# Kernel tuning notes

Measured on AMD Instinct MI355X. Metric: run time of the kernel, lower is better.

## Reference

```python
import jax, jax.numpy as jnp
import numpy as np

QP_ITERS = 500          # projected-gradient iterations on the dual (converges for this tiny QP)
S_PEN = 1000.0          # slack penalty from the cvxpy objective
BN_EPS = 1e-5


def batchnorm(x, gamma, beta):
    # x: (B, N, C); BatchNorm1d training-mode stats over (batch, points)
    mu = x.mean(axis=(0, 1))
    var = x.var(axis=(0, 1))
    return (x - mu) * jax.lax.rsqrt(var + BN_EPS) * gamma + beta


def solve_qp(p, G, h):
    # min_z,s 0.5||z-p||^2 + 1000||s||^2  s.t. G z <= h + s, s >= 0
    # Dual (eliminating z = p - G^T lam, s = lam/(2*1000)):
    #   min_{lam>=0} 0.5 lam^T M lam - lam^T q,  M = G G^T + I/(2*S_PEN), q = G p - h
    nc = G.shape[1]
    M = jnp.einsum('bcv,bdv->bcd', G, G) + jnp.eye(nc, dtype=G.dtype) / (2.0 * S_PEN)
    q = jnp.einsum('bcv,bv->bc', G, p) - h
    # safe step size: 1/trace(M) <= 1/lambda_max(M)
    alpha = jax.lax.stop_gradient(1.0 / jnp.trace(M, axis1=1, axis2=2))[:, None]

    def step(lam, _):
        grad = jnp.einsum('bcd,bd->bc', M, lam) - q
        return jnp.maximum(lam - alpha * grad, 0.0), None

    lam0 = jnp.zeros_like(q)
    lam, _ = jax.lax.scan(step, lam0, None, length=QP_ITERS)
    z = p - jnp.einsum('bcv,bc->bv', G, lam)
    return z


def setup_inputs() -> dict:
    key = jax.random.key(0)
    ks = jax.random.split(key, 16)
    B, N, NC = 64, 8192, 12

    def w(k, shape, s):
        return (jax.random.normal(k, shape) * s).astype(jnp.float32)

    bc2 = jnp.concatenate([w(ks[10], (NC * 3,), 0.02), jnp.full((NC,), 0.02, jnp.float32)])
    return {
        'pcd': jax.random.normal(ks[0], (B, N, 3), dtype=jnp.float32),
        # MiniPointNet (1x1 convs as matmuls) + batchnorm affine params
        'W1': w(ks[1], (64, 3), 0.4), 'b1': jnp.zeros(64), 'g1': jnp.ones(64), 'be1': jnp.zeros(64),
        'W2': w(ks[2], (128, 64), 0.1), 'b2': jnp.zeros(128), 'g2': jnp.ones(128), 'be2': jnp.zeros(128),
        'W3': w(ks[3], (256, 128), 0.07), 'b3': jnp.zeros(256), 'g3': jnp.ones(256), 'be3': jnp.zeros(256),
        'Wfc': w(ks[4], (128, 256), 0.05), 'bfc': jnp.zeros(128),
        # constraint_net: 128 -> 128 -> 48
        'Wc1': w(ks[5], (128, 128), 0.08), 'bc1': jnp.zeros(128),
        'Wc2': w(ks[6], (NC * 4, 128), 0.08), 'bc2': bc2,
        # p_net: 128 -> 64 -> 7 (last layer ~N(0, 0.001), zero bias)
        'Wp1': w(ks[7], (64, 128), 0.08), 'bp1': jnp.zeros(64),
        'Wp2': w(ks[8], (7, 64), 0.001), 'bp2': jnp.zeros(7),
    }


def reference(pcd, W1, b1, g1, be1, W2, b2, g2, be2, W3, b3, g3, be3,
              Wfc, bfc, Wc1, bc1, Wc2, bc2, Wp1, bp1, Wp2, bp2):
    B = pcd.shape[0]
    NC = bc2.shape[0] // 4
    # MiniPointNet: pointwise MLP + global max pool
    x = jax.nn.relu(batchnorm(pcd @ W1.T + b1, g1, be1))     # (B,N,64)
    x = jax.nn.relu(batchnorm(x @ W2.T + b2, g2, be2))       # (B,N,128)
    x = jax.nn.relu(batchnorm(x @ W3.T + b3, g3, be3))       # (B,N,256)
    feats = x.max(axis=1) @ Wfc.T + bfc                       # (B,128)

    raw_p = jax.nn.relu(feats @ Wp1.T + bp1) @ Wp2.T + bp2    # (B,7)
    p_pred = jnp.concatenate([
        jnp.tanh(raw_p[:, :3]) * 0.1,
        jnp.tanh(raw_p[:, 3:6]) * 1.57,
        jnp.tanh(raw_p[:, 6:7]) * 0.05], axis=1)

    out_cons = (jax.nn.relu(feats @ Wc1.T + bc1) @ Wc2.T + bc2).reshape(B, NC, 4)
    normals = out_cons[:, :, :3]
    # F.normalize(p=2, dim=2): clamp norm at 1e-12
    normals = normals / jnp.clip(jnp.linalg.norm(normals, axis=2, keepdims=True), 1e-12)
    h = jax.nn.softplus(out_cons[:, :, 3]) + 0.005            # (B,NC)
    G = jnp.concatenate([normals, jnp.zeros((B, NC, 4), normals.dtype)], axis=2)  # (B,NC,7)

    delta_norm = solve_qp(p_pred, G, h)                       # (B,7)
    return delta_norm, normals, h, p_pred
```

## Files before the change

kernel.cpp:

```cpp
#include <hip/hip_runtime.h>
#include <hip/hip_bf16.h>

#define NPTS 524288
#define NBATCH 64
#define NSAMP 131072

typedef __attribute__((ext_vector_type(8))) short bf16x8;
typedef __attribute__((ext_vector_type(4))) float f32x4;
typedef const float* __restrict__ fp;

__device__ __forceinline__ __hip_bfloat16 f2b(float v) { return __float2bfloat16(v); }
__device__ __forceinline__ unsigned bfbits(float v) {
    union { __hip_bfloat16 h; unsigned short s; } u; u.h = f2b(v); return (unsigned)u.s;
}
__device__ __forceinline__ unsigned pk2(float a, float b) {
    return bfbits(a) | (bfbits(b) << 16);
}
__device__ __forceinline__ float lo2f(unsigned u) { return __uint_as_float(u << 16); }
__device__ __forceinline__ float hi2f(unsigned u) { return __uint_as_float(u & 0xffff0000u); }

__device__ __forceinline__ unsigned fkey(float f) {
    unsigned u = __float_as_uint(f);
    return u ^ ((u & 0x80000000u) ? 0xFFFFFFFFu : 0x80000000u);
}
__device__ __forceinline__ float funkey(unsigned k) {
    unsigned u = (k & 0x80000000u) ? (k ^ 0x80000000u) : ~k;
    return __uint_as_float(u);
}

union U8 { bf16x8 v; __hip_bfloat16 e[8]; unsigned u[4]; };

static __device__ __forceinline__ f32x4 mfma16(bf16x8 a, bf16x8 b, f32x4 c) {
    return __builtin_amdgcn_mfma_f32_16x16x32_bf16(a, b, c, 0, 0, 0);
}

__launch_bounds__(256)
__global__ void k_setup(fp pcd, float* __restrict__ mom,
                        fp W2, fp W3, __hip_bfloat16* __restrict__ W2b,
                        __hip_bfloat16* __restrict__ W3b)
{
    if (blockIdx.x >= 1024) {
        const int i = (blockIdx.x - 1024) * 256 + threadIdx.x;
        if (i < 8192) W2b[i] = f2b(W2[i]);
        const int j = i - 8192;
        if (j >= 0 && j < 32768) W3b[j] = f2b(W3[j]);
        return;
    }
    float s[9];
#pragma unroll
    for (int i = 0; i < 9; ++i) s[i] = 0.f;
    for (int p = blockIdx.x * 256 + threadIdx.x; p < NPTS; p += 262144) {
        const float x = pcd[3*p+0], y = pcd[3*p+1], z = pcd[3*p+2];
        s[0] += x; s[1] += y; s[2] += z;
        s[3] = fmaf(x, x, s[3]); s[4] = fmaf(x, y, s[4]); s[5] = fmaf(x, z, s[5]);
        s[6] = fmaf(y, y, s[6]); s[7] = fmaf(y, z, s[7]); s[8] = fmaf(z, z, s[8]);
    }
#pragma unroll
    for (int off = 1; off < 64; off <<= 1) {
#pragma unroll
        for (int i = 0; i < 9; ++i) s[i] += __shfl_xor(s[i], off);
    }
    __shared__ float red[4][9];
    const int lane = threadIdx.x & 63, wv = threadIdx.x >> 6;
    if (lane == 0) {
#pragma unroll
        for (int i = 0; i < 9; ++i) red[wv][i] = s[i];
    }
    __syncthreads();
    if (threadIdx.x < 9) {
        const int i = threadIdx.x;
        atomicAdd(&mom[i], red[0][i] + red[1][i] + red[2][i] + red[3][i]);
    }
}

__global__ void k_fin1(const float* __restrict__ mom, fp W1, fp b1, fp g1, fp be1,
                       unsigned* __restrict__ W1p)
{
    const int c = threadIdx.x;
    const float inv = 1.f / (float)NPTS;
    const float m0 = mom[0]*inv, m1 = mom[1]*inv, m2 = mom[2]*inv;
    const float c00 = mom[3]*inv - m0*m0, c01 = mom[4]*inv - m0*m1, c02 = mom[5]*inv - m0*m2;
    const float c11 = mom[6]*inv - m1*m1, c12 = mom[7]*inv - m1*m2, c22 = mom[8]*inv - m2*m2;
    const float w0 = W1[c*3+0], w1 = W1[c*3+1], w2 = W1[c*3+2];
    const float mu = w0*m0 + w1*m1 + w2*m2 + b1[c];
    float var = w0*w0*c00 + w1*w1*c11 + w2*w2*c22 + 2.f*(w0*w1*c01 + w0*w2*c02 + w1*w2*c12);
    var = fmaxf(var, 0.f);
    const float sc = g1[c] * rsqrtf(var + 1e-5f);
    const float sh = be1[c] - mu*sc;
    W1p[c*2+0] = pk2(w0*sc, w1*sc);
    W1p[c*2+1] = pk2(w2*sc, b1[c]*sc + sh);
}

#define L1_DIRECT(a2f, px, py, pz)                                              \
    {                                                                           \
        _Pragma("unroll")                                                       \
        for (int ks = 0; ks < 2; ++ks) {                                        \
            _Pragma("unroll")                                                   \
            for (int t2 = 0; t2 < 4; ++t2) {                                    \
                const int t0 = ks*8 + 2*t2;                                     \
                float v0 = fmaf(px, lo2f(wA[t0]), hi2f(wB[t0]));                \
                v0 = fmaf(py, hi2f(wA[t0]), v0);                                \
                v0 = fmaf(pz, lo2f(wB[t0]), v0);                                \
                float v1 = fmaf(px, lo2f(wA[t0+1]), hi2f(wB[t0+1]));            \
                v1 = fmaf(py, hi2f(wA[t0+1]), v1);                              \
                v1 = fmaf(pz, lo2f(wB[t0+1]), v1);                              \
                a2f[ks].u[t2] = pk2(fmaxf(v0, 0.f), fmaxf(v1, 0.f));            \
            }                                                                   \
        }                                                                       \
    }

#define LOAD_W1()                                                               \
    unsigned wA[16], wB[16];                                                    \
    _Pragma("unroll")                                                           \
    for (int t = 0; t < 16; ++t) {                                              \
        const int ch = (t >> 3)*32 + q*8 + (t & 7);                             \
        wA[t] = W1p[ch*2]; wB[t] = W1p[ch*2+1];                                 \
    }

__launch_bounds__(256, 3)
__global__ void k_pass1(fp pcd, const unsigned* __restrict__ W1p,
                        const __hip_bfloat16* __restrict__ W2b,
                        float* __restrict__ st2s, float* __restrict__ st2q)
{
    __shared__ float red[1024];
    const int tid = threadIdx.x, wv = tid >> 6, lane = tid & 63;
    const int m = lane & 15, q = lane >> 4;
    const int batch = blockIdx.x >> 3, sub = blockIdx.x & 7;

    LOAD_W1()
    bf16x8 wb2[8][2];
#pragma unroll
    for (int nt = 0; nt < 8; ++nt) {
#pragma unroll
        for (int kk = 0; kk < 2; ++kk)
            wb2[nt][kk] = *(const bf16x8*)(W2b + (nt*16+m)*64 + kk*32 + q*8);
    }

    float s_acc[8], q_acc[8];
#pragma unroll
    for (int nt = 0; nt < 8; ++nt) { s_acc[nt] = 0.f; q_acc[nt] = 0.f; }

#pragma unroll
    for (int it = 0; it < 4; ++it) {
        const int p0 = batch*8192 + sub*1024 + it*256 + wv*16;
        const float* pp = pcd + (size_t)(p0 + m) * 3;
        const float px = pp[0], py = pp[1], pz = pp[2];
        U8 a2f[2];
        L1_DIRECT(a2f, px, py, pz)
#pragma unroll
        for (int nt = 0; nt < 8; ++nt) {
            f32x4 c = mfma16(a2f[0].v, wb2[nt][0], (f32x4){0.f,0.f,0.f,0.f});
            c = mfma16(a2f[1].v, wb2[nt][1], c);
            s_acc[nt] += (c[0] + c[1]) + (c[2] + c[3]);
            q_acc[nt] = fmaf(c[0],c[0], fmaf(c[1],c[1], fmaf(c[2],c[2], fmaf(c[3],c[3], q_acc[nt]))));
        }
    }
#pragma unroll
    for (int nt = 0; nt < 8; ++nt) {
        s_acc[nt] += __shfl_xor(s_acc[nt], 16); q_acc[nt] += __shfl_xor(q_acc[nt], 16);
        s_acc[nt] += __shfl_xor(s_acc[nt], 32); q_acc[nt] += __shfl_xor(q_acc[nt], 32);
    }
    if (q == 0) {
#pragma unroll
        for (int nt = 0; nt < 8; ++nt) {
            red[wv*128 + nt*16 + m] = s_acc[nt];
            red[512 + wv*128 + nt*16 + m] = q_acc[nt];
        }
    }
    __syncthreads();
    if (tid < 128) {
        float s = 0.f, ss = 0.f;
#pragma unroll
        for (int w4 = 0; w4 < 4; ++w4) { s += red[w4*128 + tid]; ss += red[512 + w4*128 + tid]; }
        const int slot = blockIdx.x & 63;
        atomicAdd(&st2s[slot*128 + tid], s);
        atomicAdd(&st2q[slot*128 + tid], ss);
    }
}

__global__ void k_fin2(const float* __restrict__ sum, const float* __restrict__ sq,
                       fp W2, fp g, fp be,
                       float* __restrict__ tOut, __hip_bfloat16* __restrict__ W2s)
{
    const int ch = threadIdx.x;
    float s = 0.f, ss = 0.f;
    for (int slot = 0; slot < 64; ++slot) { s += sum[slot*128 + ch]; ss += sq[slot*128 + ch]; }
    const float inv = 1.f / (float)NSAMP;
    const float mu = s * inv;
    const float var = fmaxf(ss * inv - mu*mu, 0.f);
    const float sc = g[ch] * rsqrtf(var + 1e-5f);
    tOut[ch] = be[ch] - mu*sc;
    for (int k = 0; k < 64; ++k) W2s[ch*64 + k] = f2b(sc * W2[ch*64 + k]);
}

__launch_bounds__(256)
__global__ void k_pass2(fp pcd, const unsigned* __restrict__ W1p,
                        const __hip_bfloat16* __restrict__ W2s,
                        const float* __restrict__ t2,
                        const __hip_bfloat16* __restrict__ W3b,
                        float* __restrict__ st3s, float* __restrict__ st3q,
                        unsigned* __restrict__ maxk, unsigned* __restrict__ mink)
{
    __shared__ alignas(16) __hip_bfloat16 x2s[128*136];
    __shared__ alignas(16) __hip_bfloat16 w2s[128*72];
    const int tid = threadIdx.x, wv = tid >> 6, lane = tid & 63;
    const int m = lane & 15, q = lane >> 4;
    const int batch = blockIdx.x >> 5, sub = blockIdx.x & 31;

    {
        const int row = tid >> 1, half = tid & 1;
#pragma unroll
        for (int jj = 0; jj < 2; ++jj) {
            const bf16x8 wa = *(const bf16x8*)(W2s + row*64 + half*32 + jj*16);
            const bf16x8 wb = *(const bf16x8*)(W2s + row*64 + half*32 + jj*16 + 8);
            *(bf16x8*)&w2s[row*72 + half*32 + jj*16]     = wa;
            *(bf16x8*)&w2s[row*72 + half*32 + jj*16 + 8] = wb;
        }
    }

    LOAD_W1()
    float t2v[8];
#pragma unroll
    for (int nt = 0; nt < 8; ++nt) t2v[nt] = t2[nt*16+m];

    bf16x8 wb3[4][4];
#pragma unroll
    for (int nt = 0; nt < 4; ++nt) {
        const int ch3 = wv*64 + nt*16 + m;
#pragma unroll
        for (int ks = 0; ks < 4; ++ks)
            wb3[nt][ks] = *(const bf16x8*)(W3b + ch3*128 + ks*32 + q*8);
    }

    float s3[4], q3[4], mx3[4], mn3[4];
#pragma unroll
    for (int nt = 0; nt < 4; ++nt) { s3[nt]=0.f; q3[nt]=0.f; mx3[nt]=-3.4e38f; mn3[nt]=3.4e38f; }

    __syncthreads();

#pragma unroll
    for (int half = 0; half < 2; ++half) {
        if (half) __syncthreads();
#pragma unroll
        for (int it = 0; it < 2; ++it) {
            const int p0 = batch*8192 + sub*256 + (half*2+it)*64 + wv*16;
            const float* pp = pcd + (size_t)(p0 + m) * 3;
            const float px = pp[0], py = pp[1], pz = pp[2];
            U8 a2f[2];
            L1_DIRECT(a2f, px, py, pz)
#pragma unroll
            for (int nt = 0; nt < 8; ++nt) {
                const bf16x8 wb20 = *(const bf16x8*)&w2s[(nt*16+m)*72 + 0  + q*8];
                const bf16x8 wb21 = *(const bf16x8*)&w2s[(nt*16+m)*72 + 32 + q*8];
                f32x4 c = mfma16(a2f[0].v, wb20, (f32x4){0.f,0.f,0.f,0.f});
                c = mfma16(a2f[1].v, wb21, c);
#pragma unroll
                for (int r = 0; r < 4; ++r) {
                    const float v = fmaxf(c[r] + t2v[nt], 0.f);
                    const unsigned own = bfbits(v);
                    const unsigned oth = (unsigned)__shfl_xor((int)own, 1);
                    if ((m & 1) == 0) {
                        const int row = it*64 + wv*16 + q*4 + r;
                        *(unsigned*)&x2s[row*136 + nt*16 + m] = own | (oth << 16);
                    }
                }
            }
        }
        __syncthreads();
        for (int ms = 0; ms < 8; ++ms) {
            const int rowM = (ms*16 + m) * 136;
            bf16x8 a3[4];
#pragma unroll
            for (int ks = 0; ks < 4; ++ks)
                a3[ks] = *(const bf16x8*)&x2s[rowM + ks*32 + q*8];
#pragma unroll
            for (int nt = 0; nt < 4; ++nt) {
                f32x4 c = mfma16(a3[0], wb3[nt][0], (f32x4){0.f,0.f,0.f,0.f});
                c = mfma16(a3[1], wb3[nt][1], c);
                c = mfma16(a3[2], wb3[nt][2], c);
                c = mfma16(a3[3], wb3[nt][3], c);
                s3[nt] += (c[0] + c[1]) + (c[2] + c[3]);
                q3[nt] = fmaf(c[0],c[0], fmaf(c[1],c[1], fmaf(c[2],c[2], fmaf(c[3],c[3], q3[nt]))));
                mx3[nt] = fmaxf(fmaxf(c[0], c[1]), fmaxf(fmaxf(c[2], c[3]), mx3[nt]));
                mn3[nt] = fminf(fminf(c[0], c[1]), fminf(fminf(c[2], c[3]), mn3[nt]));
            }
        }
    }
#pragma unroll
    for (int nt = 0; nt < 4; ++nt) {
        s3[nt] += __shfl_xor(s3[nt], 16);  q3[nt] += __shfl_xor(q3[nt], 16);
        mx3[nt] = fmaxf(mx3[nt], __shfl_xor(mx3[nt], 16));
        mn3[nt] = fminf(mn3[nt], __shfl_xor(mn3[nt], 16));
        s3[nt] += __shfl_xor(s3[nt], 32);  q3[nt] += __shfl_xor(q3[nt], 32);
        mx3[nt] = fmaxf(mx3[nt], __shfl_xor(mx3[nt], 32));
        mn3[nt] = fminf(mn3[nt], __shfl_xor(mn3[nt], 32));
    }
    if (q == 0) {
        const int slot = blockIdx.x & 63;
#pragma unroll
        for (int nt = 0; nt < 4; ++nt) {
            const int ch3 = wv*64 + nt*16 + m;
            atomicAdd(&st3s[slot*256 + ch3], s3[nt]);
            atomicAdd(&st3q[slot*256 + ch3], q3[nt]);
            atomicMax(&maxk[batch*256 + ch3], fkey(mx3[nt]));
            atomicMin(&mink[batch*256 + ch3], fkey(mn3[nt]));
        }
    }
}

__launch_bounds__(128)
__global__ void k_head(const float* __restrict__ st3s, const float* __restrict__ st3q,
                       fp g3, fp be3,
                       const unsigned* __restrict__ maxk, const unsigned* __restrict__ mink,
                       fp Wfc, fp bfc, fp Wc1, fp bc1, fp Wc2, fp bc2,
                       fp Wp1, fp bp1, fp Wp2, fp bp2,
                       float* __restrict__ out)
{
    __shared__ float pf[256], ft[128], hcs[128], hps[64], ocs[48], nrm[36], hS[12], pp[8];
    const int bb = blockIdx.x, tid = threadIdx.x;
#pragma unroll
    for (int h = 0; h < 2; ++h) {
        const int ch = tid + h*128;
        float s = 0.f, ss = 0.f;
        for (int slot = 0; slot < 64; ++slot) { s += st3s[slot*256 + ch]; ss += st3q[slot*256 + ch]; }
        const float inv = 1.f / (float)NPTS;
        const float mu = s * inv;
        const float var = fmaxf(ss * inv - mu*mu, 0.f);
        const float sc = g3[ch] * rsqrtf(var + 1e-5f);
        const float sh = be3[ch] - mu*sc;
        const float pick = (sc >= 0.f) ? funkey(maxk[bb*256 + ch]) : funkey(mink[bb*256 + ch]);
        pf[ch] = fmaxf(fmaf(pick, sc, sh), 0.f);
    }
    __syncthreads();
    {
        float a = bfc[tid];
        const float* wr = Wfc + tid*256;
        for (int k = 0; k < 256; ++k) a = fmaf(pf[k], wr[k], a);
        ft[tid] = a;
    }
    __syncthreads();
    {
        float a = bc1[tid];
        const float* wr = Wc1 + tid*128;
        for (int k = 0; k < 128; ++k) a = fmaf(ft[k], wr[k], a);
        hcs[tid] = fmaxf(a, 0.f);
    }
    if (tid < 64) {
        float a = bp1[tid];
        const float* wr = Wp1 + tid*128;
        for (int k = 0; k < 128; ++k) a = fmaf(ft[k], wr[k], a);
        hps[tid] = fmaxf(a, 0.f);
    }
    __syncthreads();
    if (tid < 48) {
        float a = bc2[tid];
        const float* wr = Wc2 + tid*128;
        for (int k = 0; k < 128; ++k) a = fmaf(hcs[k], wr[k], a);
        ocs[tid] = a;
    }
    if (tid < 7) {
        float a = bp2[tid];
        const float* wr = Wp2 + tid*64;
        for (int k = 0; k < 64; ++k) a = fmaf(hps[k], wr[k], a);
        const float sc = (tid < 3) ? 0.1f : ((tid < 6) ? 1.57f : 0.05f);
        pp[tid] = tanhf(a) * sc;
    }
    __syncthreads();
    if (tid < 12) {
        float nx = ocs[tid*4+0], ny = ocs[tid*4+1], nz = ocs[tid*4+2];
        const float nn = fmaxf(sqrtf(nx*nx + ny*ny + nz*nz), 1e-12f);
        const float inv = 1.f / nn;
        nx *= inv; ny *= inv; nz *= inv;
        nrm[tid*3+0] = nx; nrm[tid*3+1] = ny; nrm[tid*3+2] = nz;
        const float xx = ocs[tid*4+3];
        hS[tid] = ((xx > 20.f) ? xx : log1pf(expf(xx))) + 0.005f;
    }
    __syncthreads();

    const int lane = tid & 63;
    const int c = (lane < 12) ? lane : 11;
    const float n0 = nrm[c*3+0], n1 = nrm[c*3+1], n2 = nrm[c*3+2];
    float Mrow[12];
    float trace = 0.f;
#pragma unroll
    for (int d = 0; d < 12; ++d) {
        const float d0 = nrm[d*3+0], d1 = nrm[d*3+1], d2 = nrm[d*3+2];
        Mrow[d] = n0*d0 + n1*d1 + n2*d2 + ((d == lane) ? 5e-4f : 0.f);
        trace += d0*d0 + d1*d1 + d2*d2;
    }
    const float alpha = 1.f / (trace + 12.f*5e-4f);
    const float qc = n0*pp[0] + n1*pp[1] + n2*pp[2] - hS[c];
    float lam = 0.f;
    for (int it = 0; it < 500; ++it) {
        const float l0 = __shfl(lam, 0),  l1 = __shfl(lam, 1),  l2 = __shfl(lam, 2);
        const float l3 = __shfl(lam, 3),  l4 = __shfl(lam, 4),  l5 = __shfl(lam, 5);
        const float l6 = __shfl(lam, 6),  l7 = __shfl(lam, 7),  l8 = __shfl(lam, 8);
        const float l9 = __shfl(lam, 9),  l10 = __shfl(lam, 10), l11 = __shfl(lam, 11);
        const float g0 = fmaf(Mrow[0], l0, fmaf(Mrow[3], l3, fmaf(Mrow[6], l6, Mrow[9]*l9)));
        const float g1 = fmaf(Mrow[1], l1, fmaf(Mrow[4], l4, fmaf(Mrow[7], l7, Mrow[10]*l10)));
        const float g2 = fmaf(Mrow[2], l2, fmaf(Mrow[5], l5, fmaf(Mrow[8], l8, Mrow[11]*l11)));
        lam = fmaxf(fmaf(-alpha, g0 + g1 + g2 - qc, lam), 0.f);
    }
    float v0 = (lane < 12) ? n0*lam : 0.f;
    float v1 = (lane < 12) ? n1*lam : 0.f;
    float v2 = (lane < 12) ? n2*lam : 0.f;
#pragma unroll
    for (int off = 1; off <= 8; off <<= 1) {
        v0 += __shfl_xor(v0, off);
        v1 += __shfl_xor(v1, off);
        v2 += __shfl_xor(v2, off);
    }
    if (tid < 7) {
        float z;
        if (tid == 0) z = pp[0] - v0;
        else if (tid == 1) z = pp[1] - v1;
        else if (tid == 2) z = pp[2] - v2;
        else z = pp[tid];
        out[bb*7 + tid] = z;
    }
    if (tid < 36) out[448 + bb*36 + tid] = nrm[tid];
    if (tid < 12) out[2752 + bb*12 + tid] = hS[tid];
    if (tid < 7)  out[3520 + bb*7 + tid] = pp[tid];
}

extern "C" void kernel_launch(void* const* d_in, const int* in_sizes, int n_in,
                              void* d_out, int out_size, void* d_ws, size_t ws_size,
                              hipStream_t stream) {
    fp pcd = (fp)d_in[0];
    fp W1 = (fp)d_in[1],  b1 = (fp)d_in[2],  g1 = (fp)d_in[3],  be1 = (fp)d_in[4];
    fp W2 = (fp)d_in[5],  g2 = (fp)d_in[7],  be2 = (fp)d_in[8];
    fp W3 = (fp)d_in[9],  g3 = (fp)d_in[11], be3 = (fp)d_in[12];
    fp Wfc = (fp)d_in[13], bfc = (fp)d_in[14];
    fp Wc1 = (fp)d_in[15], bc1 = (fp)d_in[16];
    fp Wc2 = (fp)d_in[17], bc2 = (fp)d_in[18];
    fp Wp1 = (fp)d_in[19], bp1 = (fp)d_in[20];
    fp Wp2 = (fp)d_in[21], bp2 = (fp)d_in[22];

    float* ws = (float*)d_ws;
    float* mom  = ws + 0;
    float* t2   = ws + 272;
    float* st2s = ws + 400;
    float* st2q = ws + 8592;
    float* st3s = ws + 16784;
    float* st3q = ws + 33168;
    unsigned* maxk = (unsigned*)(ws + 49552);
    unsigned* mink = (unsigned*)(ws + 65936);
    __hip_bfloat16* W2b = (__hip_bfloat16*)(ws + 82320);
    __hip_bfloat16* W3b = (__hip_bfloat16*)(ws + 86416);
    unsigned* W1p = (unsigned*)(ws + 102800);
    __hip_bfloat16* W2s = (__hip_bfloat16*)(ws + 102928);
    if (ws_size < (size_t)107024 * 4) return;

    hipMemsetAsync(d_ws, 0, (size_t)65936 * 4, stream);
    hipMemsetAsync((void*)mink, 0xFF, (size_t)16384 * 4, stream);

    k_setup<<<1184, 256, 0, stream>>>(pcd, mom, W2, W3, W2b, W3b);
    k_fin1<<<1, 64, 0, stream>>>(mom, W1, b1, g1, be1, W1p);
    k_pass1<<<512, 256, 0, stream>>>(pcd, W1p, W2b, st2s, st2q);
    k_fin2<<<1, 128, 0, stream>>>(st2s, st2q, W2, g2, be2, t2, W2s);
    k_pass2<<<2048, 256, 0, stream>>>(pcd, W1p, W2s, t2, W3b,
                                      st3s, st3q, maxk, mink);
    k_head<<<64, 128, 0, stream>>>(st3s, st3q, g3, be3, maxk, mink,
                                   Wfc, bfc, Wc1, bc1, Wc2, bc2,
                                   Wp1, bp1, Wp2, bp2, (float*)d_out);
}
```

Baseline: 330.8 us.

## Fold BN3 gamma sign into W3 to drop min tracking; keep W2 in registers

Pre-multiplies W3 rows by the sign of gamma3 so the layer-3 max pool only needs per-channel maxima, removing min tracking, the min atomics and the extra memset. W2 fragments are now held in registers instead of being staged through LDS. All 256 point rows are buffered in LDS before layer 3 to remove an intermediate barrier, and launch bounds request two blocks per CU. This trades higher VGPR and LDS use for fewer atomics, fewer LDS reads and fewer syncs.

```diff
diff --git a/kernel.cpp b/kernel.cpp
--- a/kernel.cpp
+++ b/kernel.cpp
@@ -36,14 +36,18 @@
 
 __launch_bounds__(256)
 __global__ void k_setup(fp pcd, float* __restrict__ mom,
-                        fp W2, fp W3, __hip_bfloat16* __restrict__ W2b,
+                        fp W2, fp W3, fp g3,
+                        __hip_bfloat16* __restrict__ W2b,
                         __hip_bfloat16* __restrict__ W3b)
 {
     if (blockIdx.x >= 1024) {
         const int i = (blockIdx.x - 1024) * 256 + threadIdx.x;
         if (i < 8192) W2b[i] = f2b(W2[i]);
         const int j = i - 8192;
-        if (j >= 0 && j < 32768) W3b[j] = f2b(W3[j]);
+        if (j >= 0 && j < 32768) {
+            const float s = (g3[j >> 7] < 0.f) ? -1.f : 1.f;
+            W3b[j] = f2b(s * W3[j]);
+        }
         return;
     }
     float s[9];
@@ -193,32 +197,27 @@
     for (int k = 0; k < 64; ++k) W2s[ch*64 + k] = f2b(sc * W2[ch*64 + k]);
 }
 
-__launch_bounds__(256)
+__launch_bounds__(256, 2)
 __global__ void k_pass2(fp pcd, const unsigned* __restrict__ W1p,
                         const __hip_bfloat16* __restrict__ W2s,
                         const float* __restrict__ t2,
                         const __hip_bfloat16* __restrict__ W3b,
                         float* __restrict__ st3s, float* __restrict__ st3q,
-                        unsigned* __restrict__ maxk, unsigned* __restrict__ mink)
-{
-    __shared__ alignas(16) __hip_bfloat16 x2s[128*136];
-    __shared__ alignas(16) __hip_bfloat16 w2s[128*72];
+                        unsigned* __restrict__ maxk)
+{
+    __shared__ alignas(16) __hip_bfloat16 x2s[256*136];
     const int tid = threadIdx.x, wv = tid >> 6, lane = tid & 63;
     const int m = lane & 15, q = lane >> 4;
     const int batch = blockIdx.x >> 5, sub = blockIdx.x & 31;
 
-    {
-        const int row = tid >> 1, half = tid & 1;
-#pragma unroll
-        for (int jj = 0; jj < 2; ++jj) {
-            const bf16x8 wa = *(const bf16x8*)(W2s + row*64 + half*32 + jj*16);
-            const bf16x8 wb = *(const bf16x8*)(W2s + row*64 + half*32 + jj*16 + 8);
-            *(bf16x8*)&w2s[row*72 + half*32 + jj*16]     = wa;
-            *(bf16x8*)&w2s[row*72 + half*32 + jj*16 + 8] = wb;
-        }
-    }
-
     LOAD_W1()
+    bf16x8 wb2[8][2];
+#pragma unroll
+    for (int nt = 0; nt < 8; ++nt) {
+#pragma unroll
+        for (int kk = 0; kk < 2; ++kk)
+            wb2[nt][kk] = *(const bf16x8*)(W2s + (nt*16+m)*64 + kk*32 + q*8);
+    }
     float t2v[8];
 #pragma unroll
     for (int nt = 0; nt < 8; ++nt) t2v[nt] = t2[nt*16+m];
@@ -232,68 +231,58 @@
             wb3[nt][ks] = *(const bf16x8*)(W3b + ch3*128 + ks*32 + q*8);
     }
 
-    float s3[4], q3[4], mx3[4], mn3[4];
-#pragma unroll
-    for (int nt = 0; nt < 4; ++nt) { s3[nt]=0.f; q3[nt]=0.f; mx3[nt]=-3.4e38f; mn3[nt]=3.4e38f; }
-
-    __syncthreads();
-
-#pragma unroll
-    for (int half = 0; half < 2; ++half) {
-        if (half) __syncthreads();
-#pragma unroll
-        for (int it = 0; it < 2; ++it) {
-            const int p0 = batch*8192 + sub*256 + (half*2+it)*64 + wv*16;
-            const float* pp = pcd + (size_t)(p0 + m) * 3;
-            const float px = pp[0], py = pp[1], pz = pp[2];
-            U8 a2f[2];
-            L1_DIRECT(a2f, px, py, pz)
-#pragma unroll
-            for (int nt = 0; nt < 8; ++nt) {
-                const bf16x8 wb20 = *(const bf16x8*)&w2s[(nt*16+m)*72 + 0  + q*8];
-                const bf16x8 wb21 = *(const bf16x8*)&w2s[(nt*16+m)*72 + 32 + q*8];
-                f32x4 c = mfma16(a2f[0].v, wb20, (f32x4){0.f,0.f,0.f,0.f});
-                c = mfma16(a2f[1].v, wb21, c);
-#pragma unroll
-                for (int r = 0; r < 4; ++r) {
-                    const float v = fmaxf(c[r] + t2v[nt], 0.f);
-                    const unsigned own = bfbits(v);
-                    const unsigned oth = (unsigned)__shfl_xor((int)own, 1);
-                    if ((m & 1) == 0) {
-                        const int row = it*64 + wv*16 + q*4 + r;
-                        *(unsigned*)&x2s[row*136 + nt*16 + m] = own | (oth << 16);
-                    }
+#pragma unroll
+    for (int it = 0; it < 4; ++it) {
+        const int p0 = batch*8192 + sub*256 + it*64 + wv*16;
+        const float* pp = pcd + (size_t)(p0 + m) * 3;
+        const float px = pp[0], py = pp[1], pz = pp[2];
+        U8 a2f[2];
+        L1_DIRECT(a2f, px, py, pz)
+#pragma unroll
+        for (int nt = 0; nt < 8; ++nt) {
+            f32x4 c = mfma16(a2f[0].v, wb2[nt][0], (f32x4){0.f,0.f,0.f,0.f});
+            c = mfma16(a2f[1].v, wb2[nt][1], c);
+#pragma unroll
+            for (int r = 0; r < 4; ++r) {
+                const float v = fmaxf(c[r] + t2v[nt], 0.f);
+                const unsigned own = bfbits(v);
+                const unsigned oth = (unsigned)__shfl_xor((int)own, 1);
+                if ((m & 1) == 0) {
+                    const int row = it*64 + wv*16 + q*4 + r;
+                    *(unsigned*)&x2s[row*136 + nt*16 + m] = own | (oth << 16);
                 }
             }
         }
-        __syncthreads();
-        for (int ms = 0; ms < 8; ++ms) {
-            const int rowM = (ms*16 + m) * 136;
-            bf16x8 a3[4];
-#pragma unroll
-            for (int ks = 0; ks < 4; ++ks)
-                a3[ks] = *(const bf16x8*)&x2s[rowM + ks*32 + q*8];
-#pragma unroll
-            for (int nt = 0; nt < 4; ++nt) {
-                f32x4 c = mfma16(a3[0], wb3[nt][0], (f32x4){0.f,0.f,0.f,0.f});
-                c = mfma16(a3[1], wb3[nt][1], c);
-                c = mfma16(a3[2], wb3[nt][2], c);
-                c = mfma16(a3[3], wb3[nt][3], c);
-                s3[nt] += (c[0] + c[1]) + (c[2] + c[3]);
-                q3[nt] = fmaf(c[0],c[0], fmaf(c[1],c[1], fmaf(c[2],c[2], fmaf(c[3],c[3], q3[nt]))));
-                mx3[nt] = fmaxf(fmaxf(c[0], c[1]), fmaxf(fmaxf(c[2], c[3]), mx3[nt]));
-                mn3[nt] = fminf(fminf(c[0], c[1]), fminf(fminf(c[2], c[3]), mn3[nt]));
-            }
+    }
+    __syncthreads();
+
+    float s3[4], q3[4], mx3[4];
+#pragma unroll
+    for (int nt = 0; nt < 4; ++nt) { s3[nt]=0.f; q3[nt]=0.f; mx3[nt]=-3.4e38f; }
+
+    for (int ms = 0; ms < 16; ++ms) {
+        const int rowM = (ms*16 + m) * 136;
+        bf16x8 a3[4];
+#pragma unroll
+        for (int ks = 0; ks < 4; ++ks)
+            a3[ks] = *(const bf16x8*)&x2s[rowM + ks*32 + q*8];
+#pragma unroll
+        for (int nt = 0; nt < 4; ++nt) {
+            f32x4 c = mfma16(a3[0], wb3[nt][0], (f32x4){0.f,0.f,0.f,0.f});
+            c = mfma16(a3[1], wb3[nt][1], c);
+            c = mfma16(a3[2], wb3[nt][2], c);
+            c = mfma16(a3[3], wb3[nt][3], c);
+            s3[nt] += (c[0] + c[1]) + (c[2] + c[3]);
+            q3[nt] = fmaf(c[0],c[0], fmaf(c[1],c[1], fmaf(c[2],c[2], fmaf(c[3],c[3], q3[nt]))));
+            mx3[nt] = fmaxf(fmaxf(c[0], c[1]), fmaxf(fmaxf(c[2], c[3]), mx3[nt]));
         }
     }
 #pragma unroll
     for (int nt = 0; nt < 4; ++nt) {
         s3[nt] += __shfl_xor(s3[nt], 16);  q3[nt] += __shfl_xor(q3[nt], 16);
         mx3[nt] = fmaxf(mx3[nt], __shfl_xor(mx3[nt], 16));
-        mn3[nt] = fminf(mn3[nt], __shfl_xor(mn3[nt], 16));
         s3[nt] += __shfl_xor(s3[nt], 32);  q3[nt] += __shfl_xor(q3[nt], 32);
         mx3[nt] = fmaxf(mx3[nt], __shfl_xor(mx3[nt], 32));
-        mn3[nt] = fminf(mn3[nt], __shfl_xor(mn3[nt], 32));
     }
     if (q == 0) {
         const int slot = blockIdx.x & 63;
@@ -303,15 +292,13 @@
             atomicAdd(&st3s[slot*256 + ch3], s3[nt]);
             atomicAdd(&st3q[slot*256 + ch3], q3[nt]);
             atomicMax(&maxk[batch*256 + ch3], fkey(mx3[nt]));
-            atomicMin(&mink[batch*256 + ch3], fkey(mn3[nt]));
         }
     }
 }
 
 __launch_bounds__(128)
 __global__ void k_head(const float* __restrict__ st3s, const float* __restrict__ st3q,
-                       fp g3, fp be3,
-                       const unsigned* __restrict__ maxk, const unsigned* __restrict__ mink,
+                       fp g3, fp be3, const unsigned* __restrict__ maxk,
                        fp Wfc, fp bfc, fp Wc1, fp bc1, fp Wc2, fp bc2,
                        fp Wp1, fp bp1, fp Wp2, fp bp2,
                        float* __restrict__ out)
@@ -326,10 +313,9 @@
         const float inv = 1.f / (float)NPTS;
         const float mu = s * inv;
         const float var = fmaxf(ss * inv - mu*mu, 0.f);
-        const float sc = g3[ch] * rsqrtf(var + 1e-5f);
-        const float sh = be3[ch] - mu*sc;
-        const float pick = (sc >= 0.f) ? funkey(maxk[bb*256 + ch]) : funkey(mink[bb*256 + ch]);
-        pf[ch] = fmaxf(fmaf(pick, sc, sh), 0.f);
+        const float asc = fabsf(g3[ch]) * rsqrtf(var + 1e-5f);
+        const float mx = funkey(maxk[bb*256 + ch]);
+        pf[ch] = fmaxf(fmaf(asc, mx - mu, be3[ch]), 0.f);
     }
     __syncthreads();
     {
@@ -444,7 +430,6 @@
     float* st3s = ws + 16784;
     float* st3q = ws + 33168;
     unsigned* maxk = (unsigned*)(ws + 49552);
-    unsigned* mink = (unsigned*)(ws + 65936);
     __hip_bfloat16* W2b = (__hip_bfloat16*)(ws + 82320);
     __hip_bfloat16* W3b = (__hip_bfloat16*)(ws + 86416);
     unsigned* W1p = (unsigned*)(ws + 102800);
@@ -452,15 +437,14 @@
     if (ws_size < (size_t)107024 * 4) return;
 
     hipMemsetAsync(d_ws, 0, (size_t)65936 * 4, stream);
-    hipMemsetAsync((void*)mink, 0xFF, (size_t)16384 * 4, stream);
-
-    k_setup<<<1184, 256, 0, stream>>>(pcd, mom, W2, W3, W2b, W3b);
+
+    k_setup<<<1184, 256, 0, stream>>>(pcd, mom, W2, W3, g3, W2b, W3b);
     k_fin1<<<1, 64, 0, stream>>>(mom, W1, b1, g1, be1, W1p);
     k_pass1<<<512, 256, 0, stream>>>(pcd, W1p, W2b, st2s, st2q);
     k_fin2<<<1, 128, 0, stream>>>(st2s, st2q, W2, g2, be2, t2, W2s);
     k_pass2<<<2048, 256, 0, stream>>>(pcd, W1p, W2s, t2, W3b,
-                                      st3s, st3q, maxk, mink);
-    k_head<<<64, 128, 0, stream>>>(st3s, st3q, g3, be3, maxk, mink,
+                                      st3s, st3q, maxk);
+    k_head<<<64, 128, 0, stream>>>(st3s, st3q, g3, be3, maxk,
                                    Wfc, bfc, Wc1, bc1, Wc2, bc2,
                                    Wp1, bp1, Wp2, bp2, (float*)d_out);
 }
```

Result: faster. 270.0 us (-18.4%).
